# Optimization experiments

Measured on AMD Instinct MI355X. Metric: run time of the kernel, lower is better.

## Reference

```python
import jax, jax.numpy as jnp
import numpy as np

# dims
B, T, H = 4, 2048, 768
HEADS, D = 4, 768          # GATConv(out_channels=768, heads=4, concat=False)
L = 3                      # num_layers
WIN = 2
K = 2 * WIN + 1
EPS = 1e-5
NEG_SLOPE = 0.2            # PyG GATConv leaky_relu slope


def setup_inputs() -> dict:
    key = jax.random.key(0)
    ks = jax.random.split(key, 4)
    s = 1.0 / np.sqrt(H)
    x = jax.random.normal(ks[0], (B, T, H), jnp.float32)
    W = jax.random.normal(ks[1], (L, H, HEADS, D), jnp.float32) * s   # lin weights per layer
    a_src = jax.random.normal(ks[2], (L, HEADS, D), jnp.float32) * s  # att_src
    a_dst = jax.random.normal(ks[3], (L, HEADS, D), jnp.float32) * s  # att_dst
    bias = jnp.zeros((L, D), jnp.float32)                             # GATConv bias (concat=False -> [D])
    gamma = jnp.ones((L, H), jnp.float32)                             # LayerNorm weight
    beta = jnp.zeros((L, H), jnp.float32)                             # LayerNorm bias
    return {"x": x, "W": W, "a_src": a_src, "a_dst": a_dst,
            "bias": bias, "gamma": gamma, "beta": beta}


def _layernorm(z, g, b):
    m = jnp.mean(z, axis=-1, keepdims=True)
    v = jnp.mean((z - m) ** 2, axis=-1, keepdims=True)
    return (z - m) * jax.lax.rsqrt(v + EPS) * g + b


def _gat_layer(x, Wl, asrc_w, adst_w, bias_l, idx, mask):
    # x: [B,T,H]; banded GAT with neighborhoods idx: [T,K] (clipped), mask: [T,K]
    h = jnp.einsum('bti,ihd->bthd', x, Wl)                 # [B,T,heads,D]
    asrc = jnp.einsum('bthd,hd->bth', h, asrc_w)           # per-source-node score term
    adst = jnp.einsum('bthd,hd->bth', h, adst_w)           # per-target-node score term
    h_nb = h[:, idx]                                       # [B,T,K,heads,D] gathered neighbors j
    score = jax.nn.leaky_relu(asrc[:, idx] + adst[:, :, None, :], NEG_SLOPE)  # [B,T,K,heads]
    score = jnp.where(mask[None, :, :, None], score, -jnp.inf)
    attn = jax.nn.softmax(score, axis=2)                   # softmax over incoming edges per target
    out = jnp.einsum('btkh,btkhd->bthd', attn, h_nb)       # weighted aggregation
    return out.mean(axis=2) + bias_l                       # concat=False -> mean over heads


def reference(x, W, a_src, a_dst, bias, gamma, beta):
    # banded neighborhood indices (window edges both directions + self-loop from PyG default)
    offs = jnp.arange(-WIN, WIN + 1)
    idx = jnp.arange(T)[:, None] + offs[None, :]           # [T,K]
    mask = (idx >= 0) & (idx < T)
    idx = jnp.clip(idx, 0, T - 1)
    for l in range(L):
        res = x
        y = _gat_layer(x, W[l], a_src[l], a_dst[l], bias[l], idx, mask)
        x = _layernorm(y + res, gamma[l], beta[l])         # dropout = identity in eval
    return x
```

## Files before the change

### kernel.cpp

```cpp
#include <hip/hip_runtime.h>
#include <stdint.h>

#define TT 2048
#define BB 4
#define HH 768
#define NHEADS 4
#define DD 768
#define NN 3072
#define LL 3
#define BT 8192
#define KNB 5
#define NBLK 12
#define ATPB 8
#define NROWS 12
#define HSTR 3080

typedef __bf16 bf16x8 __attribute__((ext_vector_type(8)));
typedef float f32x4 __attribute__((ext_vector_type(4)));

__device__ __forceinline__ unsigned short f2bf(float f){
  union { float f; unsigned u; } v; v.f = f;
  unsigned u = v.u;
  return (unsigned short)((u + 0x7FFFu + ((u >> 16) & 1u)) >> 16);
}
__device__ __forceinline__ float bf2f(unsigned short h){
  union { unsigned u; float f; } v; v.u = ((unsigned)h) << 16;
  return v.f;
}
__device__ __forceinline__ void gload16(const unsigned short* g, unsigned short* l){
  __builtin_amdgcn_global_load_lds((const __attribute__((address_space(1))) void*)g,
                                   (__attribute__((address_space(3))) void*)l, 16, 0, 0);
}

__global__ void wt_kernel(const float* __restrict__ W, unsigned short* __restrict__ Wt){
  __shared__ float tile[32][33];
  int l = blockIdx.z;
  int n0 = blockIdx.x * 32, k0 = blockIdx.y * 32;
  int tx = threadIdx.x, ty = threadIdx.y;
  const float* Wl = W + (size_t)l * HH * NN;
  for (int r = 0; r < 4; r++)
    tile[ty + r*8][tx] = Wl[(size_t)(k0 + ty + r*8) * NN + n0 + tx];
  __syncthreads();
  unsigned short* Wtl = Wt + (size_t)l * NN * HH;
  for (int r = 0; r < 4; r++){
    int n = n0 + ty + r*8;
    Wtl[(size_t)n * HH + k0 + tx] = f2bf(tile[tx][ty + r*8]);
  }
}

__global__ void xconv_kernel(const float* __restrict__ x, unsigned short* __restrict__ xb){
  int i = blockIdx.x * blockDim.x + threadIdx.x;
  float4 v = ((const float4*)x)[i];
  ushort4 o;
  o.x = f2bf(v.x); o.y = f2bf(v.y); o.z = f2bf(v.z); o.w = f2bf(v.w);
  *(ushort4*)(xb + (size_t)i * 4) = o;
}

#define BM 128
#define BN 128
#define BK 64

__global__ __launch_bounds__(256, 2) void gemm_kernel(
    const unsigned short* __restrict__ xb,
    const unsigned short* __restrict__ wt,
    unsigned short* __restrict__ hout,
    const float* __restrict__ a_srcl,
    const float* __restrict__ a_dstl,
    float* __restrict__ psrc,
    float* __restrict__ pdst){
  __shared__ __align__(16) unsigned short xs[BM][BK];
  __shared__ __align__(16) unsigned short wsd[BN][BK];
  int bm = blockIdx.y * BM;
  int bn = blockIdx.x * BN;
  int tid = threadIdx.x;
  int wave = tid >> 6, lane = tid & 63;
  int m16 = lane & 15, q = lane >> 4;
  int wm = (wave >> 1) * 64, wn = (wave & 1) * 64;
  int r8 = lane >> 3, c8 = lane & 7;
  int cg = (c8 ^ r8) * 8;
  const unsigned short* ga[4]; const unsigned short* gb[4];
  unsigned short* la[4]; unsigned short* lb[4];
  #pragma unroll
  for (int s = 0; s < 4; s++){
    int row = wave * 32 + s * 8;
    ga[s] = xb + (size_t)(bm + row + r8) * HH + cg;
    gb[s] = wt + (size_t)(bn + row + r8) * HH + cg;
    la[s] = &xs[row][0];
    lb[s] = &wsd[row][0];
  }
  int rd0 = ((0 + q) ^ (m16 & 7)) * 8;
  int rd1 = ((4 + q) ^ (m16 & 7)) * 8;
  f32x4 acc[4][4] = {};
  for (int k0 = 0; k0 < HH; k0 += BK){
    #pragma unroll
    for (int s = 0; s < 4; s++){
      gload16(ga[s] + k0, la[s]);
      gload16(gb[s] + k0, lb[s]);
    }
    __syncthreads();
    bf16x8 af[4], bfr[4];
    for (int i = 0; i < 4; i++)
      af[i] = __builtin_bit_cast(bf16x8, *(const uint4*)(&xs[wm + i*16 + m16][rd0]));
    for (int j = 0; j < 4; j++)
      bfr[j] = __builtin_bit_cast(bf16x8, *(const uint4*)(&wsd[wn + j*16 + m16][rd0]));
    for (int i = 0; i < 4; i++)
      for (int j = 0; j < 4; j++)
        acc[i][j] = __builtin_amdgcn_mfma_f32_16x16x32_bf16(af[i], bfr[j], acc[i][j], 0, 0, 0);
    for (int i = 0; i < 4; i++)
      af[i] = __builtin_bit_cast(bf16x8, *(const uint4*)(&xs[wm + i*16 + m16][rd1]));
    for (int j = 0; j < 4; j++)
      bfr[j] = __builtin_bit_cast(bf16x8, *(const uint4*)(&wsd[wn + j*16 + m16][rd1]));
    for (int i = 0; i < 4; i++)
      for (int j = 0; j < 4; j++)
        acc[i][j] = __builtin_amdgcn_mfma_f32_16x16x32_bf16(af[i], bfr[j], acc[i][j], 0, 0, 0);
    __syncthreads();
  }
  for (int i = 0; i < 4; i++){
    int row0 = bm + wm + i*16 + q*4;
    for (int j = 0; j < 4; j++){
      int col = bn + wn + j*16 + m16;
      unsigned short* hp = hout + (size_t)row0 * NN + col;
      hp[0]            = f2bf(acc[i][j][0]);
      hp[NN]           = f2bf(acc[i][j][1]);
      hp[2*(size_t)NN] = f2bf(acc[i][j][2]);
      hp[3*(size_t)NN] = f2bf(acc[i][j][3]);
    }
  }
  int col0 = bn + wn;
  int head = col0 / DD;
  int blk  = (col0 % DD) >> 6;
  float wsrc[4], wdstw[4];
  for (int j = 0; j < 4; j++){
    int n = col0 + j*16 + m16;
    wsrc[j]  = a_srcl[n];
    wdstw[j] = a_dstl[n];
  }
  for (int i = 0; i < 4; i++){
    for (int reg = 0; reg < 4; reg++){
      float ss = 0.f, dd = 0.f;
      for (int j = 0; j < 4; j++){
        float v = acc[i][j][reg];
        ss += v * wsrc[j];
        dd += v * wdstw[j];
      }
      ss += __shfl_xor(ss, 1, 64); dd += __shfl_xor(dd, 1, 64);
      ss += __shfl_xor(ss, 2, 64); dd += __shfl_xor(dd, 2, 64);
      ss += __shfl_xor(ss, 4, 64); dd += __shfl_xor(dd, 4, 64);
      ss += __shfl_xor(ss, 8, 64); dd += __shfl_xor(dd, 8, 64);
      if (m16 == 0){
        int row = bm + wm + i*16 + q*4 + reg;
        size_t slot = (size_t)row * (NHEADS * NBLK) + head * NBLK + blk;
        psrc[slot] = ss;
        pdst[slot] = dd;
      }
    }
  }
}

__global__ __launch_bounds__(256) void srcred_kernel(
    const float* __restrict__ psrc, const float* __restrict__ pdst,
    float* __restrict__ asrc, float* __restrict__ adst){
  int task = blockIdx.x * 256 + threadIdx.x;
  const float* ps = psrc + (size_t)task * NBLK;
  const float* pd = pdst + (size_t)task * NBLK;
  float ss = 0.f, dd = 0.f;
  for (int i = 0; i < NBLK; i++){ ss += ps[i]; dd += pd[i]; }
  asrc[task] = ss;
  adst[task] = dd;
}

__global__ __launch_bounds__(768) void attn_ln_kernel(const unsigned short* __restrict__ h,
    const float* __restrict__ asrc, const float* __restrict__ adst,
    const float* __restrict__ xin_f32,
    const unsigned short* __restrict__ xin_bf,
    const float* __restrict__ bias_l,
    const float* __restrict__ gamma_l, const float* __restrict__ beta_l,
    float* __restrict__ x_out, unsigned short* __restrict__ xb_next,
    int write_f32){
  int bid = blockIdx.x;
  int grp = ((bid & 7) << 7) | (bid >> 3);
  int token0 = grp * ATPB;
  int t0 = token0 & (TT - 1);
  int bseq = token0 >> 11;
  int tid = threadIdx.x;
  int wave = tid >> 6, lane = tid & 63;
  __shared__ __align__(16) unsigned short hs[NROWS][HSTR];
  __shared__ float attn_s[ATPB][NHEADS][KNB];
  __shared__ float part_s[ATPB * 96], part_q[ATPB * 96];
  __shared__ float mv_mean[ATPB], mv_rstd[ATPB];
  int wv6 = wave % 6, jh = wave / 6;
  #pragma unroll
  for (int it = 0; it < 6; it++){
    int j = it * 2 + jh;
    int g = t0 - 2 + j;
    g = min(max(g, 0), TT - 1);
    const unsigned short* src = h + ((size_t)(bseq * TT + g)) * NN + wv6 * 512 + lane * 8;
    gload16(src, &hs[j][wv6 * 512]);
  }
  if (tid < ATPB * NHEADS){
    int ti = tid >> 2, head = tid & 3;
    int token = token0 + ti, t = t0 + ti;
    float sc[KNB];
    float mx = -3.0e38f;
    float ad = adst[token * NHEADS + head];
    for (int k = 0; k < KNB; k++){
      int tn = t + k - 2;
      if (tn >= 0 && tn < TT){
        float s = asrc[(token + k - 2) * NHEADS + head] + ad;
        s = s > 0.f ? s : 0.2f * s;
        sc[k] = s; mx = fmaxf(mx, s);
      } else sc[k] = -3.0e38f;
    }
    float den = 0.f;
    for (int k = 0; k < KNB; k++){
      float e = (sc[k] > -1.0e38f) ? __expf(sc[k] - mx) : 0.f;
      sc[k] = e; den += e;
    }
    float inv = 0.25f / den;
    for (int k = 0; k < KNB; k++) attn_s[ti][head][k] = sc[k] * inv;
  }
  __syncthreads();
  int ti = tid / 96, c = tid % 96;
  int token = token0 + ti;
  float ac[NHEADS][KNB];
  for (int hd = 0; hd < NHEADS; hd++)
    for (int k = 0; k < KNB; k++) ac[hd][k] = attn_s[ti][hd][k];
  float y8[8] = {};
  for (int hd = 0; hd < NHEADS; hd++){
    #pragma unroll
    for (int k = 0; k < KNB; k++){
      bf16x8 v = __builtin_bit_cast(bf16x8, *(const uint4*)(&hs[ti + k][hd * DD + c * 8]));
      float a = ac[hd][k];
      #pragma unroll
      for (int e = 0; e < 8; e++) y8[e] += a * (float)v[e];
    }
  }
  float xr[8], bb[8];
  if (xin_f32){
    const float4* p = (const float4*)&xin_f32[(size_t)token * HH + c * 8];
    *(float4*)&xr[0] = p[0]; *(float4*)&xr[4] = p[1];
  } else {
    uint4 u = *(const uint4*)&xin_bf[(size_t)token * HH + c * 8];
    const unsigned short* us = (const unsigned short*)&u;
    #pragma unroll
    for (int e = 0; e < 8; e++) xr[e] = bf2f(us[e]);
  }
  { const float4* p = (const float4*)&bias_l[c * 8];
    *(float4*)&bb[0] = p[0]; *(float4*)&bb[4] = p[1]; }
  float s = 0.f, sq = 0.f;
  #pragma unroll
  for (int e = 0; e < 8; e++){
    float zz = y8[e] + bb[e] + xr[e];
    y8[e] = zz; s += zz; sq += zz * zz;
  }
  part_s[tid] = s; part_q[tid] = sq;
  __syncthreads();
  if (wave < ATPB){
    float vs = part_s[wave * 96 + lane];
    float vq = part_q[wave * 96 + lane];
    if (lane < 32){
      vs += part_s[wave * 96 + 64 + lane];
      vq += part_q[wave * 96 + 64 + lane];
    }
    for (int off = 32; off > 0; off >>= 1){
      vs += __shfl_xor(vs, off, 64);
      vq += __shfl_xor(vq, off, 64);
    }
    if (lane == 0){
      float mean = vs * (1.f / HH);
      float var = vq * (1.f / HH) - mean * mean;
      mv_mean[wave] = mean;
      mv_rstd[wave] = rsqrtf(var + 1e-5f);
    }
  }
  __syncthreads();
  float mean = mv_mean[ti], rstd = mv_rstd[ti];
  float gr[8], br[8];
  { const float4* p = (const float4*)&gamma_l[c * 8];
    *(float4*)&gr[0] = p[0]; *(float4*)&gr[4] = p[1]; }
  { const float4* p = (const float4*)&beta_l[c * 8];
    *(float4*)&br[0] = p[0]; *(float4*)&br[4] = p[1]; }
  float o[8];
  #pragma unroll
  for (int e = 0; e < 8; e++)
    o[e] = (y8[e] - mean) * rstd * gr[e] + br[e];
  if (write_f32){
    float* xo = &x_out[(size_t)token * HH + c * 8];
    *(float4*)&xo[0] = *(float4*)&o[0];
    *(float4*)&xo[4] = *(float4*)&o[4];
  } else {
    unsigned short o16[8];
    #pragma unroll
    for (int e = 0; e < 8; e++) o16[e] = f2bf(o[e]);
    *(uint4*)(&xb_next[(size_t)token * HH + c * 8]) = *(uint4*)&o16[0];
  }
}

extern "C" void kernel_launch(void* const* d_in, const int* in_sizes, int n_in,
                              void* d_out, int out_size, void* d_ws, size_t ws_size,
                              hipStream_t stream) {
  const float* x     = (const float*)d_in[0];
  const float* W     = (const float*)d_in[1];
  const float* a_src = (const float*)d_in[2];
  const float* a_dst = (const float*)d_in[3];
  const float* bias  = (const float*)d_in[4];
  const float* gamma = (const float*)d_in[5];
  const float* beta  = (const float*)d_in[6];
  float* out = (float*)d_out;

  char* ws = (char*)d_ws;
  size_t off = 0;
  auto alloc = [&](size_t bytes)->char*{
    char* p = ws + off;
    off = (off + bytes + 255) & ~(size_t)255;
    return p;
  };
  unsigned short* wt   = (unsigned short*)alloc((size_t)LL * NN * HH * 2);
  unsigned short* xb   = (unsigned short*)alloc((size_t)BT * HH * 2);
  unsigned short* hbuf = (unsigned short*)alloc((size_t)BT * NN * 2);
  float* psrc  = (float*)alloc((size_t)BT * NHEADS * NBLK * 4);
  float* pdst  = (float*)alloc((size_t)BT * NHEADS * NBLK * 4);
  float* asrcb = (float*)alloc((size_t)BT * NHEADS * 4);
  float* adstb = (float*)alloc((size_t)BT * NHEADS * 4);

  wt_kernel<<<dim3(NN/32, HH/32, LL), dim3(32, 8), 0, stream>>>(W, wt);
  xconv_kernel<<<(BT * HH / 4) / 256, 256, 0, stream>>>(x, xb);

  for (int l = 0; l < LL; l++){
    gemm_kernel<<<dim3(NN / BN, BT / BM), 256, 0, stream>>>(
        xb, wt + (size_t)l * NN * HH, hbuf,
        a_src + (size_t)l * NHEADS * DD, a_dst + (size_t)l * NHEADS * DD,
        psrc, pdst);
    srcred_kernel<<<BT * NHEADS / 256, 256, 0, stream>>>(psrc, pdst, asrcb, adstb);
    attn_ln_kernel<<<BT / ATPB, 768, 0, stream>>>(hbuf, asrcb, adstb,
        (l == 0) ? x : nullptr, xb,
        bias + (size_t)l * DD, gamma + (size_t)l * HH, beta + (size_t)l * HH,
        out, xb, (l == LL - 1) ? 1 : 0);
  }
}
```

Measured before the change: 346.2 us.

## Read neighbor rows directly from global in attention kernel, drop LDS staging

The attention+LayerNorm kernel no longer stages the 12-row neighbor window of h into shared memory with async global-to-LDS loads. Each thread now reads its five neighbor rows straight from global memory, relying on L2/cache for reuse across neighboring tokens. Each thread also computes its own softmax weights redundantly, which removes the shared attention table and a barrier. Blocks shrink to 4 tokens and 384 threads, and the block swizzle is adjusted to match. This trades the staging overhead and large LDS footprint (which limits occupancy) for five times more global/L2 reads per output.

```diff
diff --git a/kernel.cpp b/kernel.cpp
--- a/kernel.cpp
+++ b/kernel.cpp
@@ -11,9 +11,7 @@
 #define BT 8192
 #define KNB 5
 #define NBLK 12
-#define ATPB 8
-#define NROWS 12
-#define HSTR 3080
+#define ATPB 4
 
 typedef __bf16 bf16x8 __attribute__((ext_vector_type(8)));
 typedef float f32x4 __attribute__((ext_vector_type(4)));
@@ -169,7 +167,7 @@
   adst[task] = dd;
 }
 
-__global__ __launch_bounds__(768) void attn_ln_kernel(const unsigned short* __restrict__ h,
+__global__ __launch_bounds__(384) void attn_ln_kernel(const unsigned short* __restrict__ h,
     const float* __restrict__ asrc, const float* __restrict__ adst,
     const float* __restrict__ xin_f32,
     const unsigned short* __restrict__ xin_bf,
@@ -178,58 +176,59 @@
     float* __restrict__ x_out, unsigned short* __restrict__ xb_next,
     int write_f32){
   int bid = blockIdx.x;
-  int grp = ((bid & 7) << 7) | (bid >> 3);
+  int grp = ((bid & 7) << 8) | (bid >> 3);
   int token0 = grp * ATPB;
-  int t0 = token0 & (TT - 1);
-  int bseq = token0 >> 11;
   int tid = threadIdx.x;
   int wave = tid >> 6, lane = tid & 63;
-  __shared__ __align__(16) unsigned short hs[NROWS][HSTR];
-  __shared__ float attn_s[ATPB][NHEADS][KNB];
+  int ti = tid / 96, c = tid % 96;
+  int token = token0 + ti;
+  int t = token & (TT - 1);
+  int bseq = token >> 11;
   __shared__ float part_s[ATPB * 96], part_q[ATPB * 96];
   __shared__ float mv_mean[ATPB], mv_rstd[ATPB];
-  int wv6 = wave % 6, jh = wave / 6;
-  #pragma unroll
-  for (int it = 0; it < 6; it++){
-    int j = it * 2 + jh;
-    int g = t0 - 2 + j;
-    g = min(max(g, 0), TT - 1);
-    const unsigned short* src = h + ((size_t)(bseq * TT + g)) * NN + wv6 * 512 + lane * 8;
-    gload16(src, &hs[j][wv6 * 512]);
-  }
-  if (tid < ATPB * NHEADS){
-    int ti = tid >> 2, head = tid & 3;
-    int token = token0 + ti, t = t0 + ti;
-    float sc[KNB];
+  float4 adv = *(const float4*)&adst[token * NHEADS];
+  float sc[KNB][NHEADS];
+  const unsigned short* rowp[KNB];
+  #pragma unroll
+  for (int k = 0; k < KNB; k++){
+    int tn = t + k - 2;
+    int tnc = min(max(tn, 0), TT - 1);
+    rowp[k] = h + ((size_t)(bseq * TT + tnc)) * NN + c * 8;
+    float4 sv = *(const float4*)&asrc[(bseq * TT + tnc) * NHEADS];
+    bool ok = (tn >= 0) && (tn < TT);
+    float* s4 = (float*)&sv;
+    float* ad4 = (float*)&adv;
+    #pragma unroll
+    for (int hd = 0; hd < NHEADS; hd++){
+      float s = s4[hd] + ad4[hd];
+      s = s > 0.f ? s : 0.2f * s;
+      sc[k][hd] = ok ? s : -3.0e38f;
+    }
+  }
+  float ac[NHEADS][KNB];
+  #pragma unroll
+  for (int hd = 0; hd < NHEADS; hd++){
     float mx = -3.0e38f;
-    float ad = adst[token * NHEADS + head];
+    #pragma unroll
+    for (int k = 0; k < KNB; k++) mx = fmaxf(mx, sc[k][hd]);
+    float den = 0.f;
+    float e[KNB];
+    #pragma unroll
     for (int k = 0; k < KNB; k++){
-      int tn = t + k - 2;
-      if (tn >= 0 && tn < TT){
-        float s = asrc[(token + k - 2) * NHEADS + head] + ad;
-        s = s > 0.f ? s : 0.2f * s;
-        sc[k] = s; mx = fmaxf(mx, s);
-      } else sc[k] = -3.0e38f;
-    }
-    float den = 0.f;
+      e[k] = (sc[k][hd] > -1.0e38f) ? __expf(sc[k][hd] - mx) : 0.f;
+      den += e[k];
+    }
+    float inv = 0.25f / den;
+    #pragma unroll
+    for (int k = 0; k < KNB; k++) ac[hd][k] = e[k] * inv;
+  }
+  float y8[8] = {};
+  #pragma unroll
+  for (int hd = 0; hd < NHEADS; hd++){
+    #pragma unroll
     for (int k = 0; k < KNB; k++){
-      float e = (sc[k] > -1.0e38f) ? __expf(sc[k] - mx) : 0.f;
-      sc[k] = e; den += e;
-    }
-    float inv = 0.25f / den;
-    for (int k = 0; k < KNB; k++) attn_s[ti][head][k] = sc[k] * inv;
-  }
-  __syncthreads();
-  int ti = tid / 96, c = tid % 96;
-  int token = token0 + ti;
-  float ac[NHEADS][KNB];
-  for (int hd = 0; hd < NHEADS; hd++)
-    for (int k = 0; k < KNB; k++) ac[hd][k] = attn_s[ti][hd][k];
-  float y8[8] = {};
-  for (int hd = 0; hd < NHEADS; hd++){
-    #pragma unroll
-    for (int k = 0; k < KNB; k++){
-      bf16x8 v = __builtin_bit_cast(bf16x8, *(const uint4*)(&hs[ti + k][hd * DD + c * 8]));
+      uint4 u = *(const uint4*)(rowp[k] + hd * DD);
+      bf16x8 v = __builtin_bit_cast(bf16x8, u);
       float a = ac[hd][k];
       #pragma unroll
       for (int e = 0; e < 8; e++) y8[e] += a * (float)v[e];
@@ -332,7 +331,7 @@
         a_src + (size_t)l * NHEADS * DD, a_dst + (size_t)l * NHEADS * DD,
         psrc, pdst);
     srcred_kernel<<<BT * NHEADS / 256, 256, 0, stream>>>(psrc, pdst, asrcb, adstb);
-    attn_ln_kernel<<<BT / ATPB, 768, 0, stream>>>(hbuf, asrcb, adstb,
+    attn_ln_kernel<<<BT / ATPB, 384, 0, stream>>>(hbuf, asrcb, adstb,
         (l == 0) ? x : nullptr, xb,
         bias + (size_t)l * DD, gamma + (size_t)l * HH, beta + (size_t)l * HH,
         out, xb, (l == LL - 1) ? 1 : 0);
```

Result: slower. 378.7 us (+9.4%).

## Fuse score partial reduction into attention kernel and halve tokens per block

Applied to the files above, without the earlier changes.

Drops the separate srcred kernel and has the attention/LayerNorm kernel sum the per-block GEMM partials for its 8-row neighbourhood straight into shared memory. The block is cut to 4 tokens with 384 threads, and the h-row staging loop is rewritten to match. This saves one launch and one global round-trip per layer, but more blocks now reload overlapping halo rows (8 rows per 4 tokens instead of 12 per 8). The remaining per-thread tail code assumes a 96-thread layout per token and must still hold with the new block shape.

```diff
diff --git a/kernel.cpp b/kernel.cpp
--- a/kernel.cpp
+++ b/kernel.cpp
@@ -11,9 +11,8 @@
 #define BT 8192
 #define KNB 5
 #define NBLK 12
-#define ATPB 8
-#define NROWS 12
-#define HSTR 3080
+#define ATPB 4
+#define NROWS 8
 
 typedef __bf16 bf16x8 __attribute__((ext_vector_type(8)));
 typedef float f32x4 __attribute__((ext_vector_type(4)));
@@ -157,20 +156,8 @@
   }
 }
 
-__global__ __launch_bounds__(256) void srcred_kernel(
+__global__ __launch_bounds__(384) void attn_ln_kernel(const unsigned short* __restrict__ h,
     const float* __restrict__ psrc, const float* __restrict__ pdst,
-    float* __restrict__ asrc, float* __restrict__ adst){
-  int task = blockIdx.x * 256 + threadIdx.x;
-  const float* ps = psrc + (size_t)task * NBLK;
-  const float* pd = pdst + (size_t)task * NBLK;
-  float ss = 0.f, dd = 0.f;
-  for (int i = 0; i < NBLK; i++){ ss += ps[i]; dd += pd[i]; }
-  asrc[task] = ss;
-  adst[task] = dd;
-}
-
-__global__ __launch_bounds__(768) void attn_ln_kernel(const unsigned short* __restrict__ h,
-    const float* __restrict__ asrc, const float* __restrict__ adst,
     const float* __restrict__ xin_f32,
     const unsigned short* __restrict__ xin_bf,
     const float* __restrict__ bias_l,
@@ -178,35 +165,48 @@
     float* __restrict__ x_out, unsigned short* __restrict__ xb_next,
     int write_f32){
   int bid = blockIdx.x;
-  int grp = ((bid & 7) << 7) | (bid >> 3);
+  int grp = ((bid & 7) << 8) | (bid >> 3);
   int token0 = grp * ATPB;
   int t0 = token0 & (TT - 1);
   int bseq = token0 >> 11;
   int tid = threadIdx.x;
   int wave = tid >> 6, lane = tid & 63;
-  __shared__ __align__(16) unsigned short hs[NROWS][HSTR];
+  __shared__ __align__(16) unsigned short hs[NROWS][NN];
   __shared__ float attn_s[ATPB][NHEADS][KNB];
+  __shared__ float as_sh[NROWS * NHEADS], ad_sh[NROWS * NHEADS];
   __shared__ float part_s[ATPB * 96], part_q[ATPB * 96];
   __shared__ float mv_mean[ATPB], mv_rstd[ATPB];
-  int wv6 = wave % 6, jh = wave / 6;
   #pragma unroll
-  for (int it = 0; it < 6; it++){
-    int j = it * 2 + jh;
+  for (int j = 0; j < NROWS; j++){
     int g = t0 - 2 + j;
     g = min(max(g, 0), TT - 1);
-    const unsigned short* src = h + ((size_t)(bseq * TT + g)) * NN + wv6 * 512 + lane * 8;
-    gload16(src, &hs[j][wv6 * 512]);
-  }
+    const unsigned short* src = h + ((size_t)(bseq * TT + g)) * NN + tid * 8;
+    gload16(src, &hs[j][wave * 512]);
+  }
+  if (tid < 2 * NROWS * NHEADS){
+    int which = tid >= NROWS * NHEADS;
+    int i = tid & (NROWS * NHEADS - 1);
+    int lt = i >> 2, head = i & 3;
+    int tcl = min(max(t0 - 2 + lt, 0), TT - 1);
+    const float* p = (which ? pdst : psrc) +
+        ((size_t)(bseq * TT + tcl) * NHEADS + head) * NBLK;
+    float4 a = *(const float4*)(p);
+    float4 b = *(const float4*)(p + 4);
+    float4 d = *(const float4*)(p + 8);
+    float s = a.x+a.y+a.z+a.w + b.x+b.y+b.z+b.w + d.x+d.y+d.z+d.w;
+    (which ? ad_sh : as_sh)[i] = s;
+  }
+  __syncthreads();
   if (tid < ATPB * NHEADS){
     int ti = tid >> 2, head = tid & 3;
-    int token = token0 + ti, t = t0 + ti;
+    int t = t0 + ti;
     float sc[KNB];
     float mx = -3.0e38f;
-    float ad = adst[token * NHEADS + head];
+    float ad = ad_sh[(ti + 2) * NHEADS + head];
     for (int k = 0; k < KNB; k++){
       int tn = t + k - 2;
       if (tn >= 0 && tn < TT){
-        float s = asrc[(token + k - 2) * NHEADS + head] + ad;
+        float s = as_sh[(ti + k) * NHEADS + head] + ad;
         s = s > 0.f ? s : 0.2f * s;
         sc[k] = s; mx = fmaxf(mx, s);
       } else sc[k] = -3.0e38f;
@@ -320,8 +320,6 @@
   unsigned short* hbuf = (unsigned short*)alloc((size_t)BT * NN * 2);
   float* psrc  = (float*)alloc((size_t)BT * NHEADS * NBLK * 4);
   float* pdst  = (float*)alloc((size_t)BT * NHEADS * NBLK * 4);
-  float* asrcb = (float*)alloc((size_t)BT * NHEADS * 4);
-  float* adstb = (float*)alloc((size_t)BT * NHEADS * 4);
 
   wt_kernel<<<dim3(NN/32, HH/32, LL), dim3(32, 8), 0, stream>>>(W, wt);
   xconv_kernel<<<(BT * HH / 4) / 256, 256, 0, stream>>>(x, xb);
@@ -331,8 +329,7 @@
         xb, wt + (size_t)l * NN * HH, hbuf,
         a_src + (size_t)l * NHEADS * DD, a_dst + (size_t)l * NHEADS * DD,
         psrc, pdst);
-    srcred_kernel<<<BT * NHEADS / 256, 256, 0, stream>>>(psrc, pdst, asrcb, adstb);
-    attn_ln_kernel<<<BT / ATPB, 768, 0, stream>>>(hbuf, asrcb, adstb,
+    attn_ln_kernel<<<BT / ATPB, 384, 0, stream>>>(hbuf, psrc, pdst,
         (l == 0) ? x : nullptr, xb,
         bias + (size_t)l * DD, gamma + (size_t)l * HH, beta + (size_t)l * HH,
         out, xb, (l == LL - 1) ? 1 : 0);
```

Measured after the change: 340.5 us. Within noise of the previous version (-1.7%).
